# Performance work log

Hardware: AMD Instinct MI355X
Metric: run time of the kernel (lower is better)

The kernel has to match this reference:

```python
import jax, jax.numpy as jnp
import numpy as np

N = 500000   # total objects across all segments
B = 8192     # number of segments (batch)
OBJ = 64     # object_size
H = 128      # hidden_size
CTX = 256    # context_size


def setup_inputs() -> dict:
    key = jax.random.key(0)
    ks = jax.random.split(key, 9)
    s = 0.05
    x = jax.random.normal(ks[0], (N, OBJ), jnp.float32)
    context = jax.random.normal(ks[1], (B, CTX), jnp.float32)
    # sorted segment ids, every segment nonempty (ragged lengths collapse to ~N/B each)
    segment_ids = (jnp.arange(N, dtype=jnp.int32) * B) // N
    W0 = jax.random.normal(ks[2], (OBJ, H), jnp.float32) * s
    b0 = jnp.zeros((H,), jnp.float32)
    W1 = jax.random.normal(ks[3], (H, H), jnp.float32) * s
    b1 = jnp.zeros((H,), jnp.float32)
    Wkv = jax.random.normal(ks[4], (H, 2 * H), jnp.float32) * s
    bkv = jnp.zeros((2 * H,), jnp.float32)
    Wq = jax.random.normal(ks[5], (CTX, H), jnp.float32) * s
    bq = jnp.zeros((H,), jnp.float32)
    gain = jnp.full((1, 1), -0.5 * np.log(H), jnp.float32)
    return dict(x=x, context=context, segment_ids=segment_ids,
                W0=W0, b0=b0, W1=W1, b1=b1, Wkv=Wkv, bkv=bkv,
                Wq=Wq, bq=bq, gain=gain)


def reference(x, context, segment_ids, W0, b0, W1, b1, Wkv, bkv, Wq, bq, gain):
    h = jax.nn.relu(x @ W0 + b0)          # [N, H]
    h = jax.nn.relu(h @ W1 + b1)          # [N, H]
    kv = h @ Wkv + bkv                    # [N, 2H]
    hsz = Wkv.shape[1] // 2
    key_, value = kv[:, :hsz], kv[:, hsz:]
    q = context @ Wq + bq                 # [B, H]
    qg = q[segment_ids]                   # gather == repeat_interleave
    logits = jnp.exp(gain)[0, 0] * jnp.sum(key_ * qg, axis=1)  # [N]
    # per-segment stable softmax
    m = jax.ops.segment_max(logits, segment_ids, num_segments=B)
    z = jnp.exp(logits - m[segment_ids])
    denom = jax.ops.segment_sum(z, segment_ids, num_segments=B)
    w = z / denom[segment_ids]            # [N]
    # per-segment softmax-weighted sum of values -> [B, H]
    embedding = jax.ops.segment_sum(w[:, None] * value, segment_ids, num_segments=B)
    return embedding, w[:, None]
```

## Files before the change

kernel.cpp:

```cpp
#include <hip/hip_runtime.h>
#include <math.h>

#define NN   500000
#define BB   8192
#define OBJ  64
#define HH   128
#define CTXD 256

typedef __attribute__((ext_vector_type(8))) short short8;
typedef __attribute__((ext_vector_type(4))) float f32x4;

#define W0HI  0
#define W0LO  8192
#define W1HI  16384
#define W1LO  32768
#define MQ_OFF  98304
#define BP_OFF  229376
#define PG_OFF  4292608
#define WS_NEED 8519680

__device__ __forceinline__ unsigned short f2bf(float f) {
    unsigned int u = __float_as_uint(f);
    u += 0x7FFFu + ((u >> 16) & 1u);
    return (unsigned short)(u >> 16);
}
__device__ __forceinline__ float bf2f(unsigned short h) {
    return __uint_as_float(((unsigned int)h) << 16);
}
__device__ __forceinline__ void split2(float v, unsigned short& hi, unsigned short& lo) {
    unsigned int u = __float_as_uint(v);
    hi = (unsigned short)(u >> 16);
    lo = f2bf(v - bf2f(hi));
}

__global__ void prep_frags(const float* __restrict__ W0,
                           const float* __restrict__ W1,
                           unsigned short* __restrict__ wsb)
{
    const int t = blockIdx.x * 256 + threadIdx.x;
    if (t >= 48 * 64) return;
    const int f = t >> 6, lane = t & 63;
    const float* W; int KS, bhi, blo, fl;
    if (f < 16) { W = W0; KS = 2; bhi = W0HI; blo = W0LO; fl = f; }
    else        { W = W1; KS = 4; bhi = W1HI; blo = W1LO; fl = f - 16; }
    const int nt = fl / KS, ks = fl - nt * KS;
    const int n  = nt * 16 + (lane & 15);
    const int k0 = ks * 32 + (lane >> 4) * 8;
    short8 h8, l8;
    #pragma unroll
    for (int j = 0; j < 8; ++j) {
        float v = W[(size_t)(k0 + j) * HH + n];
        unsigned short h, l; split2(v, h, l);
        h8[j] = (short)h; l8[j] = (short)l;
    }
    const int off = fl * 512 + lane * 8;
    *(short8*)(wsb + bhi + off) = h8;
    *(short8*)(wsb + blo + off) = l8;
}

__global__ void prep_M(const float* __restrict__ Wq,
                       const float* __restrict__ bq,
                       const float* __restrict__ Wkv,
                       float* __restrict__ M, float* __restrict__ bp)
{
    const int j = blockIdx.x;
    const int c = threadIdx.x;
    const float* wk = Wkv + (size_t)c * 2 * HH;
    const float* wq = Wq + (size_t)j * HH;
    float acc = 0.f;
    #pragma unroll 8
    for (int k = 0; k < HH; k += 4) {
        const float4 a = *(const float4*)(wq + k);
        const float4 b = *(const float4*)(wk + k);
        acc = fmaf(a.x, b.x, acc); acc = fmaf(a.y, b.y, acc);
        acc = fmaf(a.z, b.z, acc); acc = fmaf(a.w, b.w, acc);
    }
    M[(size_t)j * HH + c] = acc;
    if (j == 0) {
        float b = 0.f;
        #pragma unroll 8
        for (int k = 0; k < HH; k += 4) {
            const float4 a = *(const float4*)(bq + k);
            const float4 v = *(const float4*)(wk + k);
            b = fmaf(a.x, v.x, b); b = fmaf(a.y, v.y, b);
            b = fmaf(a.z, v.z, b); b = fmaf(a.w, v.w, b);
        }
        bp[c] = b;
    }
}

__global__ void p_gemm2(const float* __restrict__ context,
                        const float* __restrict__ M,
                        const float* __restrict__ bp,
                        float* __restrict__ pg)
{
    const int c = threadIdx.x;
    const int seg0 = blockIdx.x * 8;
    float acc[8];
    const float b = bp[c];
    #pragma unroll
    for (int s = 0; s < 8; ++s) acc[s] = b;
    #pragma unroll 4
    for (int k = 0; k < CTXD; ++k) {
        const float mv = M[(size_t)k * HH + c];
        #pragma unroll
        for (int s = 0; s < 8; ++s)
            acc[s] = fmaf(context[(size_t)(seg0 + s) * CTXD + k], mv, acc[s]);
    }
    #pragma unroll
    for (int s = 0; s < 8; ++s) pg[(size_t)(seg0 + s) * HH + c] = acc[s];
}

__launch_bounds__(512, 8)
__global__ void seg_wave(const float* __restrict__ x,
                         const float* __restrict__ context,
                         const float* __restrict__ Wq,   const float* __restrict__ bq,
                         const float* __restrict__ Wkv,  const float* __restrict__ bkv,
                         const float* __restrict__ b0,
                         const float* __restrict__ b1,
                         const float* __restrict__ gain,
                         const unsigned short* __restrict__ wsb,
                         const float* __restrict__ pg,
                         float* __restrict__ out_emb, float* __restrict__ out_w)
{
    __shared__ __align__(16) unsigned short h0f[2 * 64 * 128];
    __shared__ __align__(16) float psum_t[8][64];
    __shared__ __align__(16) float wvs[64];
    __shared__ float uu[HH];
    __shared__ float qv[HH];

    const int tid  = threadIdx.x;
    const int w    = tid >> 6;
    const int lane = tid & 63;
    const int seg  = blockIdx.x;
    const int nl = lane & 15, qq = lane >> 4;
    const int ebits = 16 * (nl & 7);

    const int start = (int)(((long long)seg * NN + BB - 1) / BB);
    const int end   = (int)(((long long)(seg + 1) * NN + BB - 1) / BB);
    const int count = end - start;

    if (!pg) {
        if (tid < HH) {
            float a = bq[tid];
            for (int k = 0; k < CTXD; ++k)
                a = fmaf(context[(size_t)seg * CTXD + k], Wq[(size_t)k * HH + tid], a);
            qv[tid] = a;
        }
        __syncthreads();
    }

    {
        const int ks = w >> 2, mt = w & 3;
        int row = start + mt * 16 + nl;
        if (row > NN - 1) row = NN - 1;
        const float* xp = x + (size_t)row * OBJ + ks * 32 + qq * 8;
        const float4 a0 = *(const float4*)xp;
        const float4 a1 = *(const float4*)(xp + 4);
        const float vv[8] = {a0.x, a0.y, a0.z, a0.w, a1.x, a1.y, a1.z, a1.w};
        short8 h8, l8;
        #pragma unroll
        for (int j = 0; j < 8; ++j) {
            unsigned short h, l; split2(vv[j], h, l);
            h8[j] = (short)h; l8[j] = (short)l;
        }
        *(short8*)&h0f[((0 * 2 + ks) * 4 + mt) * 512 + lane * 8] = h8;
        *(short8*)&h0f[((1 * 2 + ks) * 4 + mt) * 512 + lane * 8] = l8;
    }
    __syncthreads();

    float pv;
    if (pg) {
        pv = pg[(size_t)seg * HH + w * 16 + nl];
    } else {
        const int c = w * 16 + nl;
        float s = 0.f;
        for (int k = 0; k < HH; ++k)
            s = fmaf(Wkv[(size_t)c * 2 * HH + k], qv[k], s);
        pv = s;
    }

    f32x4 a1acc[4];
    #pragma unroll
    for (int mt = 0; mt < 4; ++mt) a1acc[mt] = {0.f, 0.f, 0.f, 0.f};
    #pragma unroll
    for (int ks = 0; ks < 2; ++ks) {
        const int fb = (w * 2 + ks) * 512 + lane * 8;
        const short8 bh = *(const short8*)(wsb + W0HI + fb);
        const short8 bl = *(const short8*)(wsb + W0LO + fb);
        short8 ah[4], al[4];
        #pragma unroll
        for (int mt = 0; mt < 4; ++mt) {
            ah[mt] = *(const short8*)&h0f[((0 * 2 + ks) * 4 + mt) * 512 + lane * 8];
            al[mt] = *(const short8*)&h0f[((1 * 2 + ks) * 4 + mt) * 512 + lane * 8];
        }
        #pragma unroll
        for (int mt = 0; mt < 4; ++mt) {
            a1acc[mt] = __builtin_amdgcn_mfma_f32_16x16x32_bf16(bh, ah[mt], a1acc[mt], 0, 0, 0);
            a1acc[mt] = __builtin_amdgcn_mfma_f32_16x16x32_bf16(bl, ah[mt], a1acc[mt], 0, 0, 0);
            a1acc[mt] = __builtin_amdgcn_mfma_f32_16x16x32_bf16(bh, al[mt], a1acc[mt], 0, 0, 0);
        }
    }
    __syncthreads();

    {
        const float4 b0v = *(const float4*)(b0 + w * 16 + qq * 4);
        const float bb[4] = {b0v.x, b0v.y, b0v.z, b0v.w};
        #pragma unroll
        for (int mt = 0; mt < 4; ++mt) {
            unsigned int hu[2], lu[2];
            #pragma unroll
            for (int pr = 0; pr < 2; ++pr) {
                unsigned short ha, la, hb, lb;
                float v0 = fmaxf(a1acc[mt][2 * pr + 0] + bb[2 * pr + 0], 0.f);
                float v1 = fmaxf(a1acc[mt][2 * pr + 1] + bb[2 * pr + 1], 0.f);
                split2(v0, ha, la);
                split2(v1, hb, lb);
                hu[pr] = (unsigned)ha | ((unsigned)hb << 16);
                lu[pr] = (unsigned)la | ((unsigned)lb << 16);
            }
            const int off = (mt * 16 + nl) * 256 + ((32 * w + 8 * qq) ^ ebits);
            *(uint2*)((char*)h0f + off)         = make_uint2(hu[0], hu[1]);
            *(uint2*)((char*)h0f + 16384 + off) = make_uint2(lu[0], lu[1]);
        }
    }
    __syncthreads();

    f32x4 acc2[4];
    #pragma unroll
    for (int mt = 0; mt < 4; ++mt) acc2[mt] = {0.f, 0.f, 0.f, 0.f};
    #pragma unroll
    for (int j = 0; j < 4; ++j) {
        short8 ah[4], al[4];
        #pragma unroll
        for (int mt = 0; mt < 4; ++mt) {
            const int off = (mt * 16 + nl) * 256 + ((64 * j + 16 * qq) ^ ebits);
            ah[mt] = *(const short8*)((const char*)h0f + off);
            al[mt] = *(const short8*)((const char*)h0f + 16384 + off);
        }
        const int fb = (w * 4 + j) * 512 + lane * 8;
        const short8 bh = *(const short8*)(wsb + W1HI + fb);
        const short8 bl = *(const short8*)(wsb + W1LO + fb);
        #pragma unroll
        for (int mt = 0; mt < 4; ++mt) {
            acc2[mt] = __builtin_amdgcn_mfma_f32_16x16x32_bf16(ah[mt], bh, acc2[mt], 0, 0, 0);
            acc2[mt] = __builtin_amdgcn_mfma_f32_16x16x32_bf16(ah[mt], bl, acc2[mt], 0, 0, 0);
            acc2[mt] = __builtin_amdgcn_mfma_f32_16x16x32_bf16(al[mt], bh, acc2[mt], 0, 0, 0);
        }
    }

    {
        const float b1v = b1[w * 16 + nl];
        #pragma unroll
        for (int mt = 0; mt < 4; ++mt)
            #pragma unroll
            for (int r = 0; r < 4; ++r)
                acc2[mt][r] = fmaxf(acc2[mt][r] + b1v, 0.f);
    }

    #pragma unroll
    for (int mt = 0; mt < 4; ++mt) {
        #pragma unroll
        for (int r = 0; r < 4; ++r) {
            float s = acc2[mt][r] * pv;
            #pragma unroll
            for (int off = 1; off <= 8; off <<= 1) s += __shfl_xor(s, off, 64);
            if (nl == 0) psum_t[w][mt * 16 + qq * 4 + r] = s;
        }
    }
    __syncthreads();

    if (w == 0) {
        const float eg2 = expf(gain[0]) * 1.44269504f;
        float s8 = psum_t[0][lane] + psum_t[1][lane] + psum_t[2][lane] + psum_t[3][lane]
                 + psum_t[4][lane] + psum_t[5][lane] + psum_t[6][lane] + psum_t[7][lane];
        float lp = (lane < count) ? eg2 * s8 : -INFINITY;
        float m = lp;
        #pragma unroll
        for (int off = 1; off <= 32; off <<= 1) m = fmaxf(m, __shfl_xor(m, off, 64));
        float ez = exp2f(lp - m);
        float Z = ez;
        #pragma unroll
        for (int off = 1; off <= 32; off <<= 1) Z += __shfl_xor(Z, off, 64);
        const float wr = ez * (1.f / Z);
        wvs[lane] = wr;
        if (lane < count) out_w[start + lane] = wr;
    }
    __syncthreads();

    {
        float s = 0.f;
        #pragma unroll
        for (int mt = 0; mt < 4; ++mt) {
            const f32x4 wv4 = *(const f32x4*)&wvs[mt * 16 + qq * 4];
            s = fmaf(acc2[mt][0], wv4[0], s);
            s = fmaf(acc2[mt][1], wv4[1], s);
            s = fmaf(acc2[mt][2], wv4[2], s);
            s = fmaf(acc2[mt][3], wv4[3], s);
        }
        s += __shfl_xor(s, 16, 64);
        s += __shfl_xor(s, 32, 64);
        if (qq == 0) uu[w * 16 + nl] = s;
    }
    __syncthreads();

    float* esum = &psum_t[0][0];
    {
        const int c = tid & 127, kh = tid >> 7;
        float e = (kh == 0) ? bkv[HH + c] : 0.f;
        f32x4 u4[8];
        #pragma unroll
        for (int i = 0; i < 8; ++i) u4[i] = *(const f32x4*)&uu[kh * 32 + i * 4];
        #pragma unroll
        for (int i = 0; i < 8; ++i)
            #pragma unroll
            for (int t = 0; t < 4; ++t)
                e = fmaf(u4[i][t], Wkv[(size_t)(kh * 32 + i * 4 + t) * 2 * HH + HH + c], e);
        esum[tid] = e;
    }
    __syncthreads();
    if (tid < HH)
        out_emb[(size_t)seg * HH + tid] =
            esum[tid] + esum[tid + 128] + esum[tid + 256] + esum[tid + 384];
}

extern "C" void kernel_launch(void* const* d_in, const int* in_sizes, int n_in,
                              void* d_out, int out_size, void* d_ws, size_t ws_size,
                              hipStream_t stream)
{
    (void)in_sizes; (void)n_in; (void)out_size;
    const float* x    = (const float*)d_in[0];
    const float* ctx  = (const float*)d_in[1];
    const float* W0   = (const float*)d_in[3];
    const float* b0   = (const float*)d_in[4];
    const float* W1   = (const float*)d_in[5];
    const float* b1   = (const float*)d_in[6];
    const float* Wkv  = (const float*)d_in[7];
    const float* bkv  = (const float*)d_in[8];
    const float* Wq   = (const float*)d_in[9];
    const float* bq   = (const float*)d_in[10];
    const float* gain = (const float*)d_in[11];

    float* out_emb = (float*)d_out;
    float* out_w   = (float*)d_out + (size_t)BB * HH;

    unsigned short* wsb = (unsigned short*)d_ws;
    const bool big_ws = (ws_size >= (size_t)WS_NEED);
    float* pg = big_ws ? (float*)((char*)d_ws + PG_OFF) : nullptr;

    hipLaunchKernelGGL(prep_frags, dim3(12), dim3(256), 0, stream, W0, W1, wsb);
    if (big_ws) {
        float* M  = (float*)((char*)d_ws + MQ_OFF);
        float* bp = (float*)((char*)d_ws + BP_OFF);
        hipLaunchKernelGGL(prep_M, dim3(256), dim3(128), 0, stream, Wq, bq, Wkv, M, bp);
        hipLaunchKernelGGL(p_gemm2, dim3(BB / 8), dim3(128), 0, stream, ctx, M, bp, pg);
    }
    hipLaunchKernelGGL(seg_wave, dim3(BB), dim3(512), 0, stream,
                       x, ctx, Wq, bq, Wkv, bkv, b0, b1, gain, wsb, pg,
                       out_emb, out_w);
}
```

Measured before the change: 344.6 us.

## Switch MLP matmuls from 16x16x32 to 32x32x16 MFMA tiles with 2x4 wave split

Both per-segment MLP layers now use 32x32x16 bf16 MFMA instead of 16x16x32. Waves are split into 2 row tiles by 4 column tiles, and the LDS fragment layout and prepacked weight fragments are rearranged to match. The logit and value reductions are rewritten for the new accumulator layout, with partial sums per row tile combined afterwards. The goal is fewer MFMA issues and fewer fragment loads per wave. The tradeoff is larger accumulators, more shuffle work in the logit reduction, and dropping the XOR swizzle that avoided LDS bank conflicts.

Result: slower. 368.9 us (+7.1%).

```diff
diff --git a/kernel.cpp b/kernel.cpp
--- a/kernel.cpp
+++ b/kernel.cpp
@@ -7,8 +7,9 @@
 #define HH   128
 #define CTXD 256
 
-typedef __attribute__((ext_vector_type(8))) short short8;
-typedef __attribute__((ext_vector_type(4))) float f32x4;
+typedef __attribute__((ext_vector_type(8)))  short short8;
+typedef __attribute__((ext_vector_type(4)))  float f32x4;
+typedef __attribute__((ext_vector_type(16))) float f32x16;
 
 #define W0HI  0
 #define W0LO  8192
@@ -40,12 +41,12 @@
     const int t = blockIdx.x * 256 + threadIdx.x;
     if (t >= 48 * 64) return;
     const int f = t >> 6, lane = t & 63;
-    const float* W; int KS, bhi, blo, fl;
-    if (f < 16) { W = W0; KS = 2; bhi = W0HI; blo = W0LO; fl = f; }
-    else        { W = W1; KS = 4; bhi = W1HI; blo = W1LO; fl = f - 16; }
-    const int nt = fl / KS, ks = fl - nt * KS;
-    const int n  = nt * 16 + (lane & 15);
-    const int k0 = ks * 32 + (lane >> 4) * 8;
+    const int l31 = lane & 31, l5 = lane >> 5;
+    const float* W; int bhi, blo, fl, nt, ks;
+    if (f < 16) { W = W0; bhi = W0HI; blo = W0LO; fl = f;      nt = fl >> 2; ks = fl & 3; }
+    else        { W = W1; bhi = W1HI; blo = W1LO; fl = f - 16; nt = fl >> 3; ks = fl & 7; }
+    const int n  = nt * 32 + l31;
+    const int k0 = ks * 16 + l5 * 8;
     short8 h8, l8;
     #pragma unroll
     for (int j = 0; j < 8; ++j) {
@@ -123,18 +124,18 @@
                          const float* __restrict__ pg,
                          float* __restrict__ out_emb, float* __restrict__ out_w)
 {
-    __shared__ __align__(16) unsigned short h0f[2 * 64 * 128];
+    __shared__ __align__(16) unsigned short h0f[32 * 512];
     __shared__ __align__(16) float psum_t[8][64];
     __shared__ __align__(16) float wvs[64];
-    __shared__ float uu[HH];
+    __shared__ __align__(16) float uupart[2][HH];
     __shared__ float qv[HH];
 
     const int tid  = threadIdx.x;
     const int w    = tid >> 6;
     const int lane = tid & 63;
     const int seg  = blockIdx.x;
-    const int nl = lane & 15, qq = lane >> 4;
-    const int ebits = 16 * (nl & 7);
+    const int l31 = lane & 31, l5 = lane >> 5;
+    const int rt = w & 1, ct = w >> 1;
 
     const int start = (int)(((long long)seg * NN + BB - 1) / BB);
     const int end   = (int)(((long long)(seg + 1) * NN + BB - 1) / BB);
@@ -151,10 +152,10 @@
     }
 
     {
-        const int ks = w >> 2, mt = w & 3;
-        int row = start + mt * 16 + nl;
+        const int srt = w >> 2, sks = w & 3;
+        int row = start + srt * 32 + l31;
         if (row > NN - 1) row = NN - 1;
-        const float* xp = x + (size_t)row * OBJ + ks * 32 + qq * 8;
+        const float* xp = x + (size_t)row * OBJ + sks * 16 + l5 * 8;
         const float4 a0 = *(const float4*)xp;
         const float4 a1 = *(const float4*)(xp + 4);
         const float vv[8] = {a0.x, a0.y, a0.z, a0.w, a1.x, a1.y, a1.z, a1.w};
@@ -164,117 +165,102 @@
             unsigned short h, l; split2(vv[j], h, l);
             h8[j] = (short)h; l8[j] = (short)l;
         }
-        *(short8*)&h0f[((0 * 2 + ks) * 4 + mt) * 512 + lane * 8] = h8;
-        *(short8*)&h0f[((1 * 2 + ks) * 4 + mt) * 512 + lane * 8] = l8;
+        *(short8*)&h0f[(srt * 4 + sks) * 512 + lane * 8]        = h8;
+        *(short8*)&h0f[4096 + (srt * 4 + sks) * 512 + lane * 8] = l8;
     }
     __syncthreads();
 
     float pv;
     if (pg) {
-        pv = pg[(size_t)seg * HH + w * 16 + nl];
+        pv = pg[(size_t)seg * HH + ct * 32 + l31];
     } else {
-        const int c = w * 16 + nl;
+        const int c = ct * 32 + l31;
         float s = 0.f;
         for (int k = 0; k < HH; ++k)
             s = fmaf(Wkv[(size_t)c * 2 * HH + k], qv[k], s);
         pv = s;
     }
 
-    f32x4 a1acc[4];
-    #pragma unroll
-    for (int mt = 0; mt < 4; ++mt) a1acc[mt] = {0.f, 0.f, 0.f, 0.f};
-    #pragma unroll
-    for (int ks = 0; ks < 2; ++ks) {
-        const int fb = (w * 2 + ks) * 512 + lane * 8;
-        const short8 bh = *(const short8*)(wsb + W0HI + fb);
-        const short8 bl = *(const short8*)(wsb + W0LO + fb);
-        short8 ah[4], al[4];
-        #pragma unroll
-        for (int mt = 0; mt < 4; ++mt) {
-            ah[mt] = *(const short8*)&h0f[((0 * 2 + ks) * 4 + mt) * 512 + lane * 8];
-            al[mt] = *(const short8*)&h0f[((1 * 2 + ks) * 4 + mt) * 512 + lane * 8];
-        }
-        #pragma unroll
-        for (int mt = 0; mt < 4; ++mt) {
-            a1acc[mt] = __builtin_amdgcn_mfma_f32_16x16x32_bf16(bh, ah[mt], a1acc[mt], 0, 0, 0);
-            a1acc[mt] = __builtin_amdgcn_mfma_f32_16x16x32_bf16(bl, ah[mt], a1acc[mt], 0, 0, 0);
-            a1acc[mt] = __builtin_amdgcn_mfma_f32_16x16x32_bf16(bh, al[mt], a1acc[mt], 0, 0, 0);
-        }
-    }
-    __syncthreads();
-
-    {
-        const float4 b0v = *(const float4*)(b0 + w * 16 + qq * 4);
-        const float bb[4] = {b0v.x, b0v.y, b0v.z, b0v.w};
-        #pragma unroll
-        for (int mt = 0; mt < 4; ++mt) {
-            unsigned int hu[2], lu[2];
-            #pragma unroll
-            for (int pr = 0; pr < 2; ++pr) {
-                unsigned short ha, la, hb, lb;
-                float v0 = fmaxf(a1acc[mt][2 * pr + 0] + bb[2 * pr + 0], 0.f);
-                float v1 = fmaxf(a1acc[mt][2 * pr + 1] + bb[2 * pr + 1], 0.f);
-                split2(v0, ha, la);
-                split2(v1, hb, lb);
-                hu[pr] = (unsigned)ha | ((unsigned)hb << 16);
-                lu[pr] = (unsigned)la | ((unsigned)lb << 16);
-            }
-            const int off = (mt * 16 + nl) * 256 + ((32 * w + 8 * qq) ^ ebits);
-            *(uint2*)((char*)h0f + off)         = make_uint2(hu[0], hu[1]);
-            *(uint2*)((char*)h0f + 16384 + off) = make_uint2(lu[0], lu[1]);
-        }
-    }
-    __syncthreads();
-
-    f32x4 acc2[4];
-    #pragma unroll
-    for (int mt = 0; mt < 4; ++mt) acc2[mt] = {0.f, 0.f, 0.f, 0.f};
-    #pragma unroll
-    for (int j = 0; j < 4; ++j) {
-        short8 ah[4], al[4];
-        #pragma unroll
-        for (int mt = 0; mt < 4; ++mt) {
-            const int off = (mt * 16 + nl) * 256 + ((64 * j + 16 * qq) ^ ebits);
-            ah[mt] = *(const short8*)((const char*)h0f + off);
-            al[mt] = *(const short8*)((const char*)h0f + 16384 + off);
-        }
-        const int fb = (w * 4 + j) * 512 + lane * 8;
+    f32x16 acc1 = {};
+    #pragma unroll
+    for (int ks = 0; ks < 4; ++ks) {
+        const int fb = (ct * 4 + ks) * 512 + lane * 8;
+        const short8 wh = *(const short8*)(wsb + W0HI + fb);
+        const short8 wl = *(const short8*)(wsb + W0LO + fb);
+        const short8 xh = *(const short8*)&h0f[(rt * 4 + ks) * 512 + lane * 8];
+        const short8 xl = *(const short8*)&h0f[4096 + (rt * 4 + ks) * 512 + lane * 8];
+        acc1 = __builtin_amdgcn_mfma_f32_32x32x16_bf16(wh, xh, acc1, 0, 0, 0);
+        acc1 = __builtin_amdgcn_mfma_f32_32x32x16_bf16(wh, xl, acc1, 0, 0, 0);
+        acc1 = __builtin_amdgcn_mfma_f32_32x32x16_bf16(wl, xh, acc1, 0, 0, 0);
+    }
+    __syncthreads();
+
+    #pragma unroll
+    for (int g = 0; g < 4; ++g) {
+        const float4 b0v = *(const float4*)(b0 + ct * 32 + g * 8 + l5 * 4);
+        unsigned int hu[2], lu[2];
+        #pragma unroll
+        for (int pr = 0; pr < 2; ++pr) {
+            unsigned short ha, la, hb, lb;
+            float v0 = fmaxf(acc1[g * 4 + 2 * pr + 0] + ((const float*)&b0v)[2 * pr + 0], 0.f);
+            float v1 = fmaxf(acc1[g * 4 + 2 * pr + 1] + ((const float*)&b0v)[2 * pr + 1], 0.f);
+            split2(v0, ha, la);
+            split2(v1, hb, lb);
+            hu[pr] = (unsigned)ha | ((unsigned)hb << 16);
+            lu[pr] = (unsigned)la | ((unsigned)lb << 16);
+        }
+        const int ks = 2 * ct + (g >> 1);
+        const int slot = l31 * 8 + (g & 1) * 256 + l5 * 4;
+        *(uint2*)&h0f[(rt * 8 + ks) * 512 + slot]        = make_uint2(hu[0], hu[1]);
+        *(uint2*)&h0f[(16 + rt * 8 + ks) * 512 + slot]   = make_uint2(lu[0], lu[1]);
+    }
+    __syncthreads();
+
+    f32x16 acc2 = {};
+    #pragma unroll
+    for (int ks = 0; ks < 8; ++ks) {
+        const short8 ah = *(const short8*)&h0f[(rt * 8 + ks) * 512 + lane * 8];
+        const short8 al = *(const short8*)&h0f[(16 + rt * 8 + ks) * 512 + lane * 8];
+        const int fb = (ct * 8 + ks) * 512 + lane * 8;
         const short8 bh = *(const short8*)(wsb + W1HI + fb);
         const short8 bl = *(const short8*)(wsb + W1LO + fb);
-        #pragma unroll
-        for (int mt = 0; mt < 4; ++mt) {
-            acc2[mt] = __builtin_amdgcn_mfma_f32_16x16x32_bf16(ah[mt], bh, acc2[mt], 0, 0, 0);
-            acc2[mt] = __builtin_amdgcn_mfma_f32_16x16x32_bf16(ah[mt], bl, acc2[mt], 0, 0, 0);
-            acc2[mt] = __builtin_amdgcn_mfma_f32_16x16x32_bf16(al[mt], bh, acc2[mt], 0, 0, 0);
-        }
-    }
-
-    {
-        const float b1v = b1[w * 16 + nl];
-        #pragma unroll
-        for (int mt = 0; mt < 4; ++mt)
+        acc2 = __builtin_amdgcn_mfma_f32_32x32x16_bf16(ah, bh, acc2, 0, 0, 0);
+        acc2 = __builtin_amdgcn_mfma_f32_32x32x16_bf16(ah, bl, acc2, 0, 0, 0);
+        acc2 = __builtin_amdgcn_mfma_f32_32x32x16_bf16(al, bh, acc2, 0, 0, 0);
+    }
+
+    {
+        const float b1v = b1[ct * 32 + l31];
+        #pragma unroll
+        for (int i = 0; i < 16; ++i)
+            acc2[i] = fmaxf(acc2[i] + b1v, 0.f);
+    }
+
+    {
+        float s[16];
+        #pragma unroll
+        for (int i = 0; i < 16; ++i) s[i] = acc2[i] * pv;
+        #pragma unroll
+        for (int off = 1; off <= 16; off <<= 1) {
             #pragma unroll
-            for (int r = 0; r < 4; ++r)
-                acc2[mt][r] = fmaxf(acc2[mt][r] + b1v, 0.f);
-    }
-
-    #pragma unroll
-    for (int mt = 0; mt < 4; ++mt) {
-        #pragma unroll
-        for (int r = 0; r < 4; ++r) {
-            float s = acc2[mt][r] * pv;
+            for (int i = 0; i < 16; ++i) s[i] += __shfl_xor(s[i], off, 64);
+        }
+        if (l31 == 0) {
             #pragma unroll
-            for (int off = 1; off <= 8; off <<= 1) s += __shfl_xor(s, off, 64);
-            if (nl == 0) psum_t[w][mt * 16 + qq * 4 + r] = s;
+            for (int i = 0; i < 16; ++i) {
+                const int row = rt * 32 + (i & 3) + 8 * (i >> 2) + 4 * l5;
+                psum_t[w][row] = s[i];
+            }
         }
     }
     __syncthreads();
 
     if (w == 0) {
         const float eg2 = expf(gain[0]) * 1.44269504f;
-        float s8 = psum_t[0][lane] + psum_t[1][lane] + psum_t[2][lane] + psum_t[3][lane]
-                 + psum_t[4][lane] + psum_t[5][lane] + psum_t[6][lane] + psum_t[7][lane];
-        float lp = (lane < count) ? eg2 * s8 : -INFINITY;
+        const int base = lane >> 5;
+        float s4 = psum_t[base][lane] + psum_t[base + 2][lane]
+                 + psum_t[base + 4][lane] + psum_t[base + 6][lane];
+        float lp = (lane < count) ? eg2 * s4 : -INFINITY;
         float m = lp;
         #pragma unroll
         for (int off = 1; off <= 32; off <<= 1) m = fmaxf(m, __shfl_xor(m, off, 64));
@@ -291,16 +277,15 @@
     {
         float s = 0.f;
         #pragma unroll
-        for (int mt = 0; mt < 4; ++mt) {
-            const f32x4 wv4 = *(const f32x4*)&wvs[mt * 16 + qq * 4];
-            s = fmaf(acc2[mt][0], wv4[0], s);
-            s = fmaf(acc2[mt][1], wv4[1], s);
-            s = fmaf(acc2[mt][2], wv4[2], s);
-            s = fmaf(acc2[mt][3], wv4[3], s);
-        }
-        s += __shfl_xor(s, 16, 64);
+        for (int g = 0; g < 4; ++g) {
+            const f32x4 wv4 = *(const f32x4*)&wvs[rt * 32 + g * 8 + l5 * 4];
+            s = fmaf(acc2[g * 4 + 0], wv4[0], s);
+            s = fmaf(acc2[g * 4 + 1], wv4[1], s);
+            s = fmaf(acc2[g * 4 + 2], wv4[2], s);
+            s = fmaf(acc2[g * 4 + 3], wv4[3], s);
+        }
         s += __shfl_xor(s, 32, 64);
-        if (qq == 0) uu[w * 16 + nl] = s;
+        if (l5 == 0) uupart[rt][ct * 32 + l31] = s;
     }
     __syncthreads();
 
@@ -310,7 +295,11 @@
         float e = (kh == 0) ? bkv[HH + c] : 0.f;
         f32x4 u4[8];
         #pragma unroll
-        for (int i = 0; i < 8; ++i) u4[i] = *(const f32x4*)&uu[kh * 32 + i * 4];
+        for (int i = 0; i < 8; ++i) {
+            const f32x4 a = *(const f32x4*)&uupart[0][kh * 32 + i * 4];
+            const f32x4 b = *(const f32x4*)&uupart[1][kh * 32 + i * 4];
+            u4[i] = a + b;
+        }
         #pragma unroll
         for (int i = 0; i < 8; ++i)
             #pragma unroll
```
